# Kernel tuning notes

Hardware: AMD Instinct MI355X
Metric: run time of the kernel (lower is better)

The kernel has to match this reference:

```python
import jax, jax.numpy as jnp
import numpy as np

KS = 5            # AdaCoF kernel size (ks)
DIL = 1           # dilation
PAD = (KS - 1) * DIL // 2   # ReplicationPad2d amount


def _adacof(frame, weight, alpha, beta):
    """AdaCoF: per-pixel adaptive deformable kernel warp.
    frame:  [B, C, H, W]
    weight/alpha/beta: [B, K2, H, W] with K2 = KS*KS (weight already softmaxed)
    out[b,c,i,j] = sum_k weight[b,k,i,j] * bilerp(frame_pad[b,c],
                     i + (k//KS)*DIL + alpha[b,k,i,j],
                     j + (k%KS)*DIL + beta[b,k,i,j])
    """
    B, C, H, W = frame.shape
    fp = jnp.pad(frame, ((0, 0), (0, 0), (PAD, PAD), (PAD, PAD)), mode='edge')
    Hp, Wp = H + 2 * PAD, W + 2 * PAD
    k = jnp.arange(KS * KS)
    dy = ((k // KS) * DIL).astype(frame.dtype)[:, None, None]   # [K2,1,1]
    dx = ((k % KS) * DIL).astype(frame.dtype)[:, None, None]
    ii = jnp.arange(H, dtype=frame.dtype)[:, None]              # [H,1]
    jj = jnp.arange(W, dtype=frame.dtype)[None, :]              # [1,W]
    y = jnp.clip(alpha + dy + ii, 0.0, Hp - 1.0)                # [B,K2,H,W]
    x = jnp.clip(beta + dx + jj, 0.0, Wp - 1.0)
    y0 = jnp.clip(jnp.floor(y), 0, Hp - 2).astype(jnp.int32)
    x0 = jnp.clip(jnp.floor(x), 0, Wp - 2).astype(jnp.int32)
    fy = (y - y0)[:, None]   # [B,1,K2,H,W]
    fx = (x - x0)[:, None]

    def gather(fpb, y0b, x0b):
        # fpb [C,Hp,Wp]; y0b/x0b [K2,H,W] -> four corners [C,K2,H,W]
        return (fpb[:, y0b, x0b], fpb[:, y0b, x0b + 1],
                fpb[:, y0b + 1, x0b], fpb[:, y0b + 1, x0b + 1])

    v00, v01, v10, v11 = jax.vmap(gather)(fp, y0, x0)  # each [B,C,K2,H,W]
    val = (v00 * (1 - fy) * (1 - fx) + v01 * (1 - fy) * fx
           + v10 * fy * (1 - fx) + v11 * fy * fx)
    return jnp.sum(weight[:, None] * val, axis=2)      # [B,C,H,W]


def setup_inputs() -> dict:
    key = jax.random.key(0)
    k1, k2, k3, k4, k5 = jax.random.split(key, 5)
    T, B, C, H, W = 2, 4, 3, 256, 256
    K2 = KS * KS
    return {
        'frames': jax.random.uniform(k1, (T, B, C, H, W), dtype=jnp.float32),
        'weights': jax.random.normal(k2, (B, T, K2, H, W), dtype=jnp.float32),
        'alphas': jax.random.normal(k3, (B, T, K2, H, W), dtype=jnp.float32),
        'betas': jax.random.normal(k4, (B, T, K2, H, W), dtype=jnp.float32),
        'occ_logits': jax.random.normal(k5, (B, T, H, W), dtype=jnp.float32),
    }


def reference(frames, weights, alphas, betas, occ_logits):
    # Subnet_weight ends with Softmax over the ks^2 channel dim.
    w = jax.nn.softmax(weights, axis=2)
    # moduleOcclusion ends with Softmax over the n_inputs (T) dim.
    occ = jax.nn.softmax(occ_logits, axis=1)
    T = frames.shape[0]
    out = jnp.zeros_like(frames[0])
    for t in range(T):  # small fixed T=2
        out = out + occ[:, t, None] * _adacof(frames[t], w[:, t], alphas[:, t], betas[:, t])
    return out
```

## Files before the change

### kernel.cpp

```cpp
#include <hip/hip_runtime.h>
#include <hip/hip_bf16.h>
#include <hip/hip_fp16.h>


#define KS 5
#define K2 25
#define PADR 2

constexpr int T_ = 2;
constexpr int B_ = 4;
constexpr int C_ = 3;
constexpr int H_ = 256;
constexpr int W_ = 256;
constexpr int HW_ = H_ * W_;
constexpr int BCHW_ = B_ * C_ * HW_;
constexpr float HP_MAX = (float)(H_ + 2 * PADR - 1);
constexpr float WP_MAX = (float)(W_ + 2 * PADR - 1);
constexpr float HP_M2 = (float)(H_ + 2 * PADR - 2);
constexpr float WP_M2 = (float)(W_ + 2 * PADR - 2);

constexpr int TILE_W = 32;
constexpr int TILE_H = 8;
constexpr int HALO   = 8;
constexpr int RPAD   = HALO + PADR;
constexpr int WROWS  = TILE_H + 21;
constexpr int WCOLS  = TILE_W + 21;
constexpr int PLANE  = WROWS * WCOLS;
constexpr int NTILE  = HW_ / (TILE_W * TILE_H);

__global__ __launch_bounds__(256) void adacof_tile(
    const float* __restrict__ frames,
    const float* __restrict__ weights,
    const float* __restrict__ alphas,
    const float* __restrict__ betas,
    const float* __restrict__ occl,
    float* __restrict__ part)
{
    __shared__ __half2 winA[PLANE];
    __shared__ __half2 win2[PLANE];

    const int bid  = blockIdx.x;
    const int b    = bid >> 9;
    const int rem  = bid & 511;
    const int t    = rem & 1;
    const int tile = rem >> 1;
    const int i0   = (tile >> 3) << 3;
    const int j0   = (tile & 7) << 5;

    const int tid = threadIdx.x;
    const int wy0 = i0 - RPAD;
    const int wx0 = j0 - RPAD;

    const float* __restrict__ fb = frames + (size_t)(t * B_ + b) * C_ * HW_;

    for (int e = tid; e < PLANE; e += 256) {
        const int wy = e / WCOLS;
        const int wx = e - wy * WCOLS;
        const int gy  = min(max(wy0 + wy, 0), H_ - 1);
        const int gx  = min(max(wx0 + wx, 0), W_ - 1);
        const int gx1 = min(max(wx0 + wx + 1, 0), W_ - 1);
        const int gr = gy << 8;
        winA[e] = __floats2half2_rn(fb[gr + gx], fb[HW_ + gr + gx]);
        win2[e] = __floats2half2_rn(fb[2 * HW_ + gr + gx], fb[2 * HW_ + gr + gx1]);
    }

    const int x = tid & 31, r = tid >> 5;
    const int i = i0 + r, j = j0 + x;
    const int ij = (i << 8) | j;

    const int btbase = ((b * T_ + t) * K2) * HW_ + ij;
    const float* __restrict__ wp = weights + btbase;
    const float* __restrict__ ap = alphas + btbase;
    const float* __restrict__ bp = betas + btbase;

    const float o_own = occl[(b * T_ + t) * HW_ + ij];
    const float o_oth = occl[(b * T_ + (1 - t)) * HW_ + ij];

    __syncthreads();

    float wsum = 0.0f, acc0 = 0.0f, acc1 = 0.0f, acc2 = 0.0f;
    const float fi = (float)i;
    const float fj = (float)j;
    const float oy = (float)(i0 - HALO);
    const float ox = (float)(j0 - HALO);

    float wgA[5], agA[5], bgA[5];
    float wgB[5], agB[5], bgB[5];

#define PREFETCH(BUF, BASE)                                                    \
    {                                                                          \
        _Pragma("unroll")                                                      \
        for (int q = 0; q < 5; ++q) {                                          \
            wg##BUF[q] = wp[((BASE) + q) * HW_];                               \
            ag##BUF[q] = ap[((BASE) + q) * HW_];                               \
            bg##BUF[q] = bp[((BASE) + q) * HW_];                               \
        }                                                                      \
    }

#define TAP5(BUF, BASE)                                                        \
    {                                                                          \
        _Pragma("unroll")                                                      \
        for (int q = 0; q < 5; ++q) {                                          \
            const int k = (BASE) + q;                                          \
            const float ew = __expf(wg##BUF[q]);                               \
            wsum += ew;                                                        \
            const int kd = k / KS;                                             \
            const float dy = (float)kd;                                        \
            const float dx = (float)(k - kd * KS);                             \
            const float y2  = fminf(fmaxf(ag##BUF[q] + (dy + fi), 0.0f), HP_MAX); \
            const float x2  = fminf(fmaxf(bg##BUF[q] + (dx + fj), 0.0f), WP_MAX); \
            const float y0f = fminf(floorf(y2), HP_M2);                        \
            const float x0f = fminf(floorf(x2), WP_M2);                        \
            const float fy  = y2 - y0f;                                        \
            const float fx  = x2 - x0f;                                        \
            const int iy = (int)(y0f - oy);                                    \
            const int ixx = (int)(x0f - ox);                                   \
            const int l  = iy * WCOLS + ixx;                                   \
            const float fyw = fy * ew;                                         \
            const float ey0 = ew - fyw;                                        \
            const float w01 = fx * ey0;                                        \
            const float w00 = ey0 - w01;                                       \
            const float w11 = fx * fyw;                                        \
            const float w10 = fyw - w11;                                       \
            const float2 p00 = __half22float2(winA[l]);                        \
            const float2 p01 = __half22float2(winA[l + 1]);                    \
            const float2 p10 = __half22float2(winA[l + WCOLS]);                \
            const float2 p11 = __half22float2(winA[l + WCOLS + 1]);            \
            const float2 q0  = __half22float2(win2[l]);                        \
            const float2 q1  = __half22float2(win2[l + WCOLS]);                \
            acc0 += w00 * p00.x + w01 * p01.x + w10 * p10.x + w11 * p11.x;     \
            acc1 += w00 * p00.y + w01 * p01.y + w10 * p10.y + w11 * p11.y;     \
            acc2 += w00 * q0.x  + w01 * q0.y  + w10 * q1.x  + w11 * q1.y;      \
        }                                                                      \
    }

    PREFETCH(A, 0)
    PREFETCH(B, 5)
    TAP5(A, 0)
    PREFETCH(A, 10)
    TAP5(B, 5)
    PREFETCH(B, 15)
    TAP5(A, 10)
    PREFETCH(A, 20)
    TAP5(B, 15)
    TAP5(A, 20)

#undef PREFETCH
#undef TAP5

    const float occw = 1.0f / (1.0f + __expf(o_oth - o_own));
    const float wscale = occw / wsum;

    float* __restrict__ pt = part + ((size_t)(t * B_ + b) * C_) * HW_ + ij;
    pt[0]       = acc0 * wscale;
    pt[HW_]     = acc1 * wscale;
    pt[2 * HW_] = acc2 * wscale;
}

__global__ void combine2(const float4* __restrict__ part, float4* __restrict__ out) {
    const int n = blockIdx.x * blockDim.x + threadIdx.x;
    const float4 p0 = part[n];
    const float4 p1 = part[n + BCHW_ / 4];
    float4 r;
    r.x = p0.x + p1.x; r.y = p0.y + p1.y; r.z = p0.z + p1.z; r.w = p0.w + p1.w;
    out[n] = r;
}

extern "C" void kernel_launch(void* const* d_in, const int* in_sizes, int n_in,
                              void* d_out, int out_size, void* d_ws, size_t ws_size,
                              hipStream_t stream) {
    const float* frames  = (const float*)d_in[0];
    const float* weights = (const float*)d_in[1];
    const float* alphas  = (const float*)d_in[2];
    const float* betas   = (const float*)d_in[3];
    const float* occl    = (const float*)d_in[4];
    float* out = (float*)d_out;
    float* part = (float*)d_ws;

    const int blocks = B_ * T_ * NTILE;
    adacof_tile<<<blocks, 256, 0, stream>>>(frames, weights, alphas, betas,
                                            occl, part);
    combine2<<<(BCHW_ / 4) / 256, 256, 0, stream>>>((const float4*)part,
                                                    (float4*)out);
}
```

Before: 38.80 us.

## Fuse both time steps into one block and drop the combine kernel

```diff
diff --git a/kernel.cpp b/kernel.cpp
--- a/kernel.cpp
+++ b/kernel.cpp
@@ -13,13 +13,12 @@
 constexpr int H_ = 256;
 constexpr int W_ = 256;
 constexpr int HW_ = H_ * W_;
-constexpr int BCHW_ = B_ * C_ * HW_;
 constexpr float HP_MAX = (float)(H_ + 2 * PADR - 1);
 constexpr float WP_MAX = (float)(W_ + 2 * PADR - 1);
 constexpr float HP_M2 = (float)(H_ + 2 * PADR - 2);
 constexpr float WP_M2 = (float)(W_ + 2 * PADR - 2);
 
-constexpr int TILE_W = 32;
+constexpr int TILE_W = 16;
 constexpr int TILE_H = 8;
 constexpr int HALO   = 8;
 constexpr int RPAD   = HALO + PADR;
@@ -28,43 +27,48 @@
 constexpr int PLANE  = WROWS * WCOLS;
 constexpr int NTILE  = HW_ / (TILE_W * TILE_H);
 
-__global__ __launch_bounds__(256) void adacof_tile(
+__global__ __launch_bounds__(256) void adacof_dual(
     const float* __restrict__ frames,
     const float* __restrict__ weights,
     const float* __restrict__ alphas,
     const float* __restrict__ betas,
     const float* __restrict__ occl,
-    float* __restrict__ part)
+    float* __restrict__ out)
 {
-    __shared__ __half2 winA[PLANE];
-    __shared__ __half2 win2[PLANE];
+    __shared__ __half2 winA[2 * PLANE];
+    __shared__ __half2 win2[2 * PLANE];
 
     const int bid  = blockIdx.x;
     const int b    = bid >> 9;
-    const int rem  = bid & 511;
-    const int t    = rem & 1;
-    const int tile = rem >> 1;
-    const int i0   = (tile >> 3) << 3;
-    const int j0   = (tile & 7) << 5;
+    const int tile = bid & 511;
+    const int ty   = tile >> 4;
+    const int tx   = tile & 15;
+    const int i0   = ty << 3;
+    const int j0   = tx << 4;
 
     const int tid = threadIdx.x;
+    const int t   = tid >> 7;
+    const int lt  = tid & 127;
+
     const int wy0 = i0 - RPAD;
     const int wx0 = j0 - RPAD;
 
     const float* __restrict__ fb = frames + (size_t)(t * B_ + b) * C_ * HW_;
+    __half2* __restrict__ wA = winA + t * PLANE;
+    __half2* __restrict__ w2 = win2 + t * PLANE;
 
-    for (int e = tid; e < PLANE; e += 256) {
+    for (int e = lt; e < PLANE; e += 128) {
         const int wy = e / WCOLS;
         const int wx = e - wy * WCOLS;
         const int gy  = min(max(wy0 + wy, 0), H_ - 1);
         const int gx  = min(max(wx0 + wx, 0), W_ - 1);
         const int gx1 = min(max(wx0 + wx + 1, 0), W_ - 1);
         const int gr = gy << 8;
-        winA[e] = __floats2half2_rn(fb[gr + gx], fb[HW_ + gr + gx]);
-        win2[e] = __floats2half2_rn(fb[2 * HW_ + gr + gx], fb[2 * HW_ + gr + gx1]);
+        wA[e] = __floats2half2_rn(fb[gr + gx], fb[HW_ + gr + gx]);
+        w2[e] = __floats2half2_rn(fb[2 * HW_ + gr + gx], fb[2 * HW_ + gr + gx1]);
     }
 
-    const int x = tid & 31, r = tid >> 5;
+    const int x = lt & 15, r = lt >> 4;
     const int i = i0 + r, j = j0 + x;
     const int ij = (i << 8) | j;
 
@@ -75,8 +79,6 @@
 
     const float o_own = occl[(b * T_ + t) * HW_ + ij];
     const float o_oth = occl[(b * T_ + (1 - t)) * HW_ + ij];
-
-    __syncthreads();
 
     float wsum = 0.0f, acc0 = 0.0f, acc1 = 0.0f, acc2 = 0.0f;
     const float fi = (float)i;
@@ -113,21 +115,21 @@
             const float x0f = fminf(floorf(x2), WP_M2);                        \
             const float fy  = y2 - y0f;                                        \
             const float fx  = x2 - x0f;                                        \
-            const int iy = (int)(y0f - oy);                                    \
+            const int iy  = (int)(y0f - oy);                                   \
             const int ixx = (int)(x0f - ox);                                   \
-            const int l  = iy * WCOLS + ixx;                                   \
+            const int l   = iy * WCOLS + ixx;                                  \
             const float fyw = fy * ew;                                         \
             const float ey0 = ew - fyw;                                        \
             const float w01 = fx * ey0;                                        \
             const float w00 = ey0 - w01;                                       \
             const float w11 = fx * fyw;                                        \
             const float w10 = fyw - w11;                                       \
-            const float2 p00 = __half22float2(winA[l]);                        \
-            const float2 p01 = __half22float2(winA[l + 1]);                    \
-            const float2 p10 = __half22float2(winA[l + WCOLS]);                \
-            const float2 p11 = __half22float2(winA[l + WCOLS + 1]);            \
-            const float2 q0  = __half22float2(win2[l]);                        \
-            const float2 q1  = __half22float2(win2[l + WCOLS]);                \
+            const float2 p00 = __half22float2(wA[l]);                          \
+            const float2 p01 = __half22float2(wA[l + 1]);                      \
+            const float2 p10 = __half22float2(wA[l + WCOLS]);                  \
+            const float2 p11 = __half22float2(wA[l + WCOLS + 1]);              \
+            const float2 q0  = __half22float2(w2[l]);                          \
+            const float2 q1  = __half22float2(w2[l + WCOLS]);                  \
             acc0 += w00 * p00.x + w01 * p01.x + w10 * p10.x + w11 * p11.x;     \
             acc1 += w00 * p00.y + w01 * p01.y + w10 * p10.y + w11 * p11.y;     \
             acc2 += w00 * q0.x  + w01 * q0.y  + w10 * q1.x  + w11 * q1.y;      \
@@ -136,6 +138,9 @@
 
     PREFETCH(A, 0)
     PREFETCH(B, 5)
+
+    __syncthreads();
+
     TAP5(A, 0)
     PREFETCH(A, 10)
     TAP5(B, 5)
@@ -150,20 +155,24 @@
 
     const float occw = 1.0f / (1.0f + __expf(o_oth - o_own));
     const float wscale = occw / wsum;
+    const float r0 = acc0 * wscale;
+    const float r1 = acc1 * wscale;
+    const float r2 = acc2 * wscale;
 
-    float* __restrict__ pt = part + ((size_t)(t * B_ + b) * C_) * HW_ + ij;
-    pt[0]       = acc0 * wscale;
-    pt[HW_]     = acc1 * wscale;
-    pt[2 * HW_] = acc2 * wscale;
-}
-
-__global__ void combine2(const float4* __restrict__ part, float4* __restrict__ out) {
-    const int n = blockIdx.x * blockDim.x + threadIdx.x;
-    const float4 p0 = part[n];
-    const float4 p1 = part[n + BCHW_ / 4];
-    float4 r;
-    r.x = p0.x + p1.x; r.y = p0.y + p1.y; r.z = p0.z + p1.z; r.w = p0.w + p1.w;
-    out[n] = r;
+    __syncthreads();
+    float* __restrict__ exch = (float*)winA;
+    if (t == 1) {
+        exch[lt * 3 + 0] = r0;
+        exch[lt * 3 + 1] = r1;
+        exch[lt * 3 + 2] = r2;
+    }
+    __syncthreads();
+    if (t == 0) {
+        float* __restrict__ op = out + (size_t)(b * C_) * HW_ + ij;
+        op[0]       = r0 + exch[lt * 3 + 0];
+        op[HW_]     = r1 + exch[lt * 3 + 1];
+        op[2 * HW_] = r2 + exch[lt * 3 + 2];
+    }
 }
 
 extern "C" void kernel_launch(void* const* d_in, const int* in_sizes, int n_in,
@@ -175,11 +184,8 @@
     const float* betas   = (const float*)d_in[3];
     const float* occl    = (const float*)d_in[4];
     float* out = (float*)d_out;
-    float* part = (float*)d_ws;
 
-    const int blocks = B_ * T_ * NTILE;
-    adacof_tile<<<blocks, 256, 0, stream>>>(frames, weights, alphas, betas,
-                                            occl, part);
-    combine2<<<(BCHW_ / 4) / 256, 256, 0, stream>>>((const float4*)part,
-                                                    (float4*)out);
+    const int blocks = B_ * NTILE;
+    adacof_dual<<<blocks, 256, 0, stream>>>(frames, weights, alphas, betas,
+                                            occl, out);
 }
```

New measurement: 58.46 us. +50.7%, slower.
